# Kernel optimization log

Hardware: AMD Instinct MI355X
Metric: run time of the kernel (lower is better)

## Reference

```python
import jax, jax.numpy as jnp
import numpy as np
from jax import lax

H = 666
W = 666
EPS = 1e-5


def _conv(x, w, b):
    # NCHW conv, SAME padding, stride 1
    y = lax.conv_general_dilated(x, w, (1, 1), 'SAME',
                                 dimension_numbers=('NCHW', 'OIHW', 'NCHW'))
    return y + b[None, :, None, None]


def _bn2d(x, g, b):
    m = jnp.mean(x, (0, 2, 3), keepdims=True)
    v = jnp.var(x, (0, 2, 3), keepdims=True)
    return (x - m) * lax.rsqrt(v + EPS) * g[None, :, None, None] + b[None, :, None, None]


def _pool(x):
    return lax.reduce_window(x, -jnp.inf, lax.max, (1, 1, 2, 2), (1, 1, 2, 2), 'VALID')


def setup_inputs() -> dict:
    key = jax.random.key(0)
    ks = jax.random.split(key, 16)
    P, N, D = 20000, 32, 9

    def rn(k, shape, scale=0.05):
        return (jax.random.normal(k, shape, jnp.float32) * scale).astype(jnp.float32)

    return {
        'pillars': jax.random.normal(ks[0], (P, N, D), jnp.float32),
        'coords': jax.random.randint(ks[1], (P, 3), 0, 666, jnp.int64 if jax.config.jax_enable_x64 else jnp.int32),
        # PillarFeatureNet
        'lin_w': rn(ks[2], (64, 9)), 'lin_b': jnp.zeros((64,), jnp.float32),
        'pfn_g': jnp.ones((64,), jnp.float32), 'pfn_b': jnp.zeros((64,), jnp.float32),
        # Backbone
        'c1_w': rn(ks[3], (64, 64, 3, 3)), 'c1_b': jnp.zeros((64,), jnp.float32),
        'bn1_g': jnp.ones((64,), jnp.float32), 'bn1_b': jnp.zeros((64,), jnp.float32),
        'c2_w': rn(ks[4], (128, 64, 3, 3)), 'c2_b': jnp.zeros((128,), jnp.float32),
        'bn2_g': jnp.ones((128,), jnp.float32), 'bn2_b': jnp.zeros((128,), jnp.float32),
        # SSD head
        'h1_w': rn(ks[5], (256, 128, 3, 3)), 'h1_b': jnp.zeros((256,), jnp.float32),
        'hbn_g': jnp.ones((256,), jnp.float32), 'hbn_b': jnp.zeros((256,), jnp.float32),
        'hb_w': rn(ks[6], (21, 256, 3, 3)), 'hb_b': jnp.zeros((21,), jnp.float32),
        'hc_w': rn(ks[7], (3, 256, 3, 3)), 'hc_b': jnp.zeros((3,), jnp.float32),
    }


def reference(pillars, coords, lin_w, lin_b, pfn_g, pfn_b,
              c1_w, c1_b, bn1_g, bn1_b, c2_w, c2_b, bn2_g, bn2_b,
              h1_w, h1_b, hbn_g, hbn_b, hb_w, hb_b, hc_w, hc_b):
    P, N, D = pillars.shape
    # --- PillarFeatureNet: Linear -> BN1d (batch stats) -> ReLU -> max over points ---
    x = pillars.reshape(P * N, D) @ lin_w.T + lin_b           # [P*N, 64]
    m = jnp.mean(x, 0)
    v = jnp.var(x, 0)
    x = jax.nn.relu((x - m) * lax.rsqrt(v + EPS) * pfn_g + pfn_b)
    feats = jnp.max(x.reshape(P, N, -1), axis=1)              # [P, 64]

    # --- PseudoImageScatter: one vectorized scatter replacing the per-pillar loop ---
    y_idx = coords[:, 1]
    x_idx = coords[:, 2]
    valid = (y_idx >= 0) & (y_idx < H) & (x_idx >= 0) & (x_idx < W)
    y_idx = jnp.where(valid, y_idx, H)   # OOB -> dropped by scatter
    x_idx = jnp.where(valid, x_idx, W)
    img = jnp.zeros((64, H, W), feats.dtype).at[:, y_idx, x_idx].set(feats.T, mode='drop')
    img = img[None]                                           # [1, 64, H, W]

    # --- Backbone ---
    b1 = _pool(jax.nn.relu(_bn2d(_conv(img, c1_w, c1_b), bn1_g, bn1_b)))   # [1,64,333,333]
    b2 = _pool(jax.nn.relu(_bn2d(_conv(b1, c2_w, c2_b), bn2_g, bn2_b)))    # [1,128,166,166]

    # --- SSD head ---
    h = jax.nn.relu(_bn2d(_conv(b2, h1_w, h1_b), hbn_g, hbn_b))            # [1,256,166,166]
    bbox = _conv(h, hb_w, hb_b)                                            # [1,21,166,166]
    cls = _conv(h, hc_w, hc_b)                                             # [1,3,166,166]
    return (bbox, cls)
```

## Files before the change

### kernel.cpp

```cpp
#include <hip/hip_runtime.h>
#include <hip/hip_bf16.h>
#include <cstdint>
#include <cstddef>

#define BN_EPS 1e-5f

typedef short short8 __attribute__((ext_vector_type(8)));
typedef float float16 __attribute__((ext_vector_type(16)));
typedef unsigned short ushort_t;

__device__ __forceinline__ float bf2f(ushort_t u) {
  return __uint_as_float(((unsigned int)u) << 16);
}
__device__ __forceinline__ ushort_t f2bf(float f) {
  unsigned int u = __float_as_uint(f);
  u += 0x7FFFu + ((u >> 16) & 1u);
  return (ushort_t)(u >> 16);
}

__device__ __forceinline__ void gload16(const ushort_t* g, ushort_t* l) {
  __builtin_amdgcn_global_load_lds(
      (const __attribute__((address_space(1))) unsigned int*)g,
      (__attribute__((address_space(3))) unsigned int*)l, 16, 0, 0);
}


__global__ __launch_bounds__(512) void pillar_moments(
    const float* __restrict__ pillars, float* __restrict__ mom) {
  float S[9], M[45];
#pragma unroll
  for (int i = 0; i < 9; ++i) S[i] = 0.f;
#pragma unroll
  for (int i = 0; i < 45; ++i) M[i] = 0.f;
  const int t = blockIdx.x * 512 + threadIdx.x;
  const int NTH = 128 * 512;
  for (long r = t; r < 640000; r += NTH) {
    float x[9];
    const float* rp = pillars + r * 9;
#pragma unroll
    for (int d = 0; d < 9; ++d) x[d] = rp[d];
    int k = 0;
#pragma unroll
    for (int i = 0; i < 9; ++i) {
      S[i] += x[i];
#pragma unroll
      for (int j = i; j < 9; ++j) { M[k] += x[i] * x[j]; ++k; }
    }
  }
#pragma unroll
  for (int i = 0; i < 9; ++i)
#pragma unroll
    for (int o = 32; o > 0; o >>= 1) S[i] += __shfl_xor(S[i], o);
#pragma unroll
  for (int i = 0; i < 45; ++i)
#pragma unroll
    for (int o = 32; o > 0; o >>= 1) M[i] += __shfl_xor(M[i], o);
  __shared__ float red[8 * 54];
  int lane = threadIdx.x & 63, wv = threadIdx.x >> 6;
  if (lane == 0) {
#pragma unroll
    for (int i = 0; i < 9; ++i) red[wv * 54 + i] = S[i];
#pragma unroll
    for (int i = 0; i < 45; ++i) red[wv * 54 + 9 + i] = M[i];
  }
  __syncthreads();
  if (threadIdx.x < 54) {
    float s = 0.f;
#pragma unroll
    for (int w8 = 0; w8 < 8; ++w8) s += red[w8 * 54 + threadIdx.x];
    atomicAdd(&mom[threadIdx.x], s);
  }
}

__global__ void pfn_finalize(const float* __restrict__ mom,
                             const float* __restrict__ lin_w,
                             const float* __restrict__ lin_b,
                             const float* __restrict__ g, const float* __restrict__ b,
                             float* __restrict__ ss) {
  int c = threadIdx.x;
  double w[9], S[9];
#pragma unroll
  for (int d = 0; d < 9; ++d) {
    w[d] = (double)lin_w[c * 9 + d];
    S[d] = (double)mom[d];
  }
  double wS = 0.0;
#pragma unroll
  for (int d = 0; d < 9; ++d) wS += w[d] * S[d];
  double wMw = 0.0;
  int k = 0;
#pragma unroll
  for (int i = 0; i < 9; ++i)
#pragma unroll
    for (int j = i; j < 9; ++j) {
      double m = (double)mom[9 + k];
      wMw += (i == j ? 1.0 : 2.0) * w[i] * w[j] * m;
      ++k;
    }
  const double N = 640000.0;
  double bc = (double)lin_b[c];
  double mean = (wS + N * bc) / N;
  double ey2 = (wMw + 2.0 * bc * wS + N * bc * bc) / N;
  double var = ey2 - mean * mean;
  if (var < 0.0) var = 0.0;
  double inv = 1.0 / sqrt(var + (double)BN_EPS);
  double sc = (double)g[c] * inv;
  ss[c] = (float)sc;
  ss[c + 64] = (float)((double)b[c] - mean * sc);
}

__global__ __launch_bounds__(256) void pfn_feats(
    const float* __restrict__ pillars, const float* __restrict__ lin_w,
    const float* __restrict__ lin_b, const float* __restrict__ ss,
    ushort_t* __restrict__ feats) {
  __shared__ float s_p[1152];
  int tid = threadIdx.x;
  int c = tid & 63, pe = tid >> 6;
  long pb = (long)blockIdx.x * 4;
  for (int i = tid; i < 1152; i += 256) s_p[i] = pillars[pb * 288 + i];
  float w[9];
#pragma unroll
  for (int d = 0; d < 9; ++d) w[d] = lin_w[c * 9 + d];
  float bl = lin_b[c];
  float sc = ss[c], sh = ss[c + 64];
  __syncthreads();
  const float* pp = &s_p[pe * 288];
  float m = -1e30f;
#pragma unroll 4
  for (int n = 0; n < 32; ++n) {
    float y = bl;
#pragma unroll
    for (int d = 0; d < 9; ++d) y += pp[n * 9 + d] * w[d];
    float v = fmaxf(y * sc + sh, 0.f);
    m = fmaxf(m, v);
  }
  feats[(pb + pe) * 64 + c] = f2bf(m);
}


__global__ void scatter_winner(const int* __restrict__ coords, int* __restrict__ winner,
                               int P) {
  int p = blockIdx.x * 256 + threadIdx.x;
  if (p >= P) return;
  int y = coords[p * 3 + 1], x = coords[p * 3 + 2];
  if (y >= 0 && y < 666 && x >= 0 && x < 666) atomicMax(&winner[y * 666 + x], p);
}


__device__ __forceinline__ void prep_one(const float* __restrict__ w,
                                         ushort_t* __restrict__ w2, int C, int N,
                                         int Ntg, int chunks, int u) {
  int total = chunks * 9 * 2 * Ntg * 64;
  if (u >= total) return;
  int l = u & 63;
  int g = u >> 6;
  int ntg = g % Ntg;
  int g2 = g / Ntg;
  int s = g2 & 1;
  int g3 = g2 >> 1;
  int pos = g3 % 9;
  int cc = g3 / 9;
  int n = ntg * 32 + (l & 31);
  int c0 = cc * 32 + s * 16 + (l >> 5) * 8;
  ushort_t o8[8];
#pragma unroll
  for (int j = 0; j < 8; ++j) {
    int c = c0 + j;
    float v = (n < N && c < C) ? w[((size_t)n * C + c) * 9 + pos] : 0.f;
    o8[j] = f2bf(v);
  }
  *(uint4*)&w2[(size_t)u * 8] = *(const uint4*)o8;
}

__device__ __forceinline__ void prep_head_one(const float* __restrict__ hb,
                                              const float* __restrict__ hc,
                                              ushort_t* __restrict__ w2, int u) {
  int total = 8 * 9 * 2 * 64;
  if (u >= total) return;
  int l = u & 63;
  int g = u >> 6;
  int s = g & 1;
  int g3 = g >> 1;
  int pos = g3 % 9;
  int cc = g3 / 9;
  int n = l & 31;
  int c0 = cc * 32 + s * 16 + (l >> 5) * 8;
  ushort_t o8[8];
#pragma unroll
  for (int j = 0; j < 8; ++j) {
    int c = c0 + j;
    float v = 0.f;
    if (n < 21) v = hb[((size_t)n * 256 + c) * 9 + pos];
    else if (n < 24) v = hc[((size_t)(n - 21) * 256 + c) * 9 + pos];
    o8[j] = f2bf(v);
  }
  *(uint4*)&w2[(size_t)u * 8] = *(const uint4*)o8;
}

__global__ void prep_all(const float* __restrict__ c1_w, const float* __restrict__ c2_w,
                         const float* __restrict__ h1_w, const float* __restrict__ hb_w,
                         const float* __restrict__ hc_w, ushort_t* __restrict__ w2c1,
                         ushort_t* __restrict__ w2c2, ushort_t* __restrict__ w2h1,
                         ushort_t* __restrict__ w2hd) {
  int b = blockIdx.x;
  int t = threadIdx.x;
  if (b < 18) prep_one(c1_w, w2c1, 64, 64, 2, 2, b * 256 + t);
  else if (b < 54) prep_one(c2_w, w2c2, 64, 128, 4, 2, (b - 18) * 256 + t);
  else if (b < 198) prep_one(h1_w, w2h1, 128, 256, 8, 4, (b - 54) * 256 + t);
  else prep_head_one(hb_w, hc_w, w2hd, (b - 198) * 256 + t);
}


__global__ void bn_make_coefs(const float* __restrict__ acc, const float* __restrict__ g,
                              const float* __restrict__ b, float invN,
                              float* __restrict__ coef, int C) {
  int c = threadIdx.x;
  if (c >= C) return;
  float m = acc[c] * invN;
  float v = fmaxf(acc[c + 256] * invN - m * m, 0.f);
  float sc = g[c] * rsqrtf(v + BN_EPS);
  coef[c] = sc;
  coef[C + c] = b[c] - m * sc;
}


__global__ __launch_bounds__(256) void bnrelu(const ushort_t* __restrict__ inp,
                                              const float* __restrict__ coef, int C,
                                              int L8, ushort_t* __restrict__ outp) {
  __shared__ float sc[512];
  int tid = threadIdx.x;
  for (int i = tid; i < 2 * C; i += 256) sc[i] = coef[i];
  __syncthreads();
  int t = blockIdx.x * 256 + tid;
  if (t >= L8) return;
  size_t e0 = (size_t)t * 8;
  int c0 = (t << 3) & (C - 1);
  short8 v = *(const short8*)&inp[e0];
  const ushort_t* vp = (const ushort_t*)&v;
  ushort_t o[8];
#pragma unroll
  for (int j = 0; j < 8; ++j) {
    float x = bf2f(vp[j]);
    o[j] = f2bf(fmaxf(x * sc[c0 + j] + sc[C + c0 + j], 0.f));
  }
  *(uint4*)&outp[e0] = *(const uint4*)o;
}


template <int NT, int WAVES, bool GATHER, bool HEAD, bool STATS, bool POOL>
__global__ __launch_bounds__(WAVES * 64, 4) void conv_mfma(
    const ushort_t* __restrict__ in, const int* __restrict__ winner,
    const ushort_t* __restrict__ feats, const ushort_t* __restrict__ w2,
    const float* __restrict__ bias, const float* __restrict__ bias2,
    const ushort_t* __restrict__ zbuf, ushort_t* __restrict__ obf,
    float* __restrict__ hpart, float* __restrict__ statacc, int W, int H, int C,
    int nchunks, int Ntg) {
  constexpr int NTHREADS = WAVES * 64;
  constexpr int NPOS = (WAVES + 2) * 66;
  constexpr int IN_U4 = NPOS * 2;
  constexpr int W_U4 = 9 * NT * 64;
  constexpr int INIT = (IN_U4 + NTHREADS - 1) / NTHREADS;
  constexpr int WIT = (W_U4 + NTHREADS - 1) / NTHREADS;
  __shared__ ushort_t s_in[2][IN_U4 * 8];
  __shared__ ushort_t s_w[2][W_U4 * 8];
  const int tid = threadIdx.x;
  const int lane = tid & 63, wv = tid >> 6;
  const int lc = lane & 31, lh = lane >> 5;
  const int x0 = blockIdx.x * 64, y0 = blockIdx.y * WAVES;
  const int z = blockIdx.z;
  const int cc0 = HEAD ? z * nchunks : 0;
  const int z_oc = HEAD ? 0 : z;

  int pc[2][3];
#pragma unroll
  for (int Mt = 0; Mt < 2; ++Mt)
#pragma unroll
    for (int kx = 0; kx < 3; ++kx) {
      int col = Mt * 32 + kx + lc;
      pc[Mt][kx] = col * 16 + (lh ^ (col & 1)) * 8;
    }

  const ushort_t* isrc[INIT];
#pragma unroll
  for (int it = 0; it < INIT; ++it) {
    isrc[it] = zbuf;
    int d = it * NTHREADS + tid;
    if (d < IN_U4) {
      int p = d >> 1, g = d & 1;
      int r = p / 66, col = p - r * 66;
      int cg = g ^ (col & 1);
      int gy = y0 - 1 + r, gx = x0 - 1 + col;
      if (gy >= 0 && gy < H && gx >= 0 && gx < W) {
        if (GATHER) {
          int pw = winner[gy * 666 + gx];
          if (pw >= 0) isrc[it] = feats + pw * 64 + cg * 8;
        } else {
          isrc[it] = in + (size_t)(gy * W + gx) * C + cg * 8;
        }
      }
    }
  }
  int wof[WIT];
#pragma unroll
  for (int it = 0; it < WIT; ++it) {
    wof[it] = 0;
    int d = it * NTHREADS + tid;
    if (d < W_U4) {
      int grp = d >> 6, l16 = d & 63;
      int pos = grp / NT, nt = grp % NT;
      wof[it] = (pos * 2 * Ntg + z_oc * NT + nt) * 512 + l16 * 8;
    }
  }

  float bv[NT];
#pragma unroll
  for (int nt = 0; nt < NT; ++nt) {
    if (HEAD) {
      bv[nt] = (z == 0) ? (lc < 21 ? bias[lc] : (lc < 24 ? bias2[lc - 21] : 0.f)) : 0.f;
    } else {
      bv[nt] = bias[(z * NT + nt) * 32 + lc];
    }
  }
  float16 acc[2][NT];
#pragma unroll
  for (int Mt = 0; Mt < 2; ++Mt)
#pragma unroll
    for (int nt = 0; nt < NT; ++nt)
#pragma unroll
      for (int r = 0; r < 16; ++r) acc[Mt][nt][r] = bv[nt];

  auto stage = [&](int ph, int b) {
    int ccg = cc0 + (ph >> 1), sh = ph & 1;
    int coff = ccg * 32 + sh * 16;
#pragma unroll
    for (int it = 0; it < INIT; ++it) {
      int d = it * NTHREADS + tid;
      if (d < IN_U4)
        gload16(isrc[it] + coff, &s_in[b][(size_t)(it * NTHREADS + wv * 64) * 8]);
    }
    int wbase = (ccg * 18 + sh) * Ntg * 512;
#pragma unroll
    for (int it = 0; it < WIT; ++it) {
      int d = it * NTHREADS + tid;
      if (d < W_U4)
        gload16(w2 + wbase + wof[it], &s_w[b][(size_t)(it * NTHREADS + wv * 64) * 8]);
    }
  };

  auto compute_phase = [&](int b) {
#pragma unroll
    for (int ky = 0; ky < 3; ++ky) {
      const ushort_t* rowp = &s_in[b][(wv + ky) * (66 * 16)];
#pragma unroll
      for (int kx = 0; kx < 3; ++kx) {
        const int pos = ky * 3 + kx;
        short8 Bf[NT];
#pragma unroll
        for (int nt = 0; nt < NT; ++nt)
          Bf[nt] = *(const short8*)&s_w[b][(pos * NT + nt) * 512 + lane * 8];
#pragma unroll
        for (int Mt = 0; Mt < 2; ++Mt) {
          short8 Af = *(const short8*)&rowp[pc[Mt][kx]];
#pragma unroll
          for (int nt = 0; nt < NT; ++nt)
            acc[Mt][nt] =
                __builtin_amdgcn_mfma_f32_32x32x16_bf16(Af, Bf[nt], acc[Mt][nt], 0, 0, 0);
        }
      }
    }
  };

  const int nph = nchunks * 2;
  stage(0, 0);
  for (int ph = 0; ph < nph; ++ph) {
    asm volatile("s_waitcnt vmcnt(0)\n\ts_barrier" ::: "memory");
    if (ph + 1 < nph) stage(ph + 1, (ph + 1) & 1);
    __builtin_amdgcn_s_setprio(1);
    compute_phase(ph & 1);
    __builtin_amdgcn_s_setprio(0);
  }

  const int y = y0 + wv;
  const bool yok = (y < H);
  const int Ntot = Ntg * 32;

  if (HEAD) {
    if (yok) {
      float* hp = hpart + (size_t)z * (size_t)(H * W) * 32;
#pragma unroll
      for (int Mt = 0; Mt < 2; ++Mt)
#pragma unroll
        for (int r = 0; r < 16; ++r) {
          int m = (r & 3) + 8 * (r >> 2) + 4 * lh;
          int x = x0 + Mt * 32 + m;
          if (x < W) {
            size_t sp = (size_t)y * W + x;
            hp[sp * 32 + lc] = acc[Mt][0][r];
          }
        }
    }
    return;
  }

  if (!POOL) {
    if (yok) {
#pragma unroll
      for (int Mt = 0; Mt < 2; ++Mt)
#pragma unroll
        for (int r = 0; r < 16; ++r) {
          int m = (r & 3) + 8 * (r >> 2) + 4 * lh;
          int x = x0 + Mt * 32 + m;
          if (x < W) {
            size_t sp = (size_t)y * W + x;
#pragma unroll
            for (int nt = 0; nt < NT; ++nt) {
              int oc = (z * NT + nt) * 32 + lc;
              obf[sp * Ntot + oc] = f2bf(acc[Mt][nt][r]);
            }
          }
        }
    }
  }

  if (STATS) {
    float s1[NT], s2[NT];
#pragma unroll
    for (int nt = 0; nt < NT; ++nt) { s1[nt] = 0.f; s2[nt] = 0.f; }
    if (yok) {
#pragma unroll
      for (int Mt = 0; Mt < 2; ++Mt)
#pragma unroll
        for (int r = 0; r < 16; ++r) {
          int m = (r & 3) + 8 * (r >> 2) + 4 * lh;
          int x = x0 + Mt * 32 + m;
          if (x < W) {
#pragma unroll
            for (int nt = 0; nt < NT; ++nt) {
              float v = acc[Mt][nt][r];
              s1[nt] += v;
              s2[nt] += v * v;
            }
          }
        }
    }
#pragma unroll
    for (int nt = 0; nt < NT; ++nt) {
      s1[nt] += __shfl_xor(s1[nt], 32);
      s2[nt] += __shfl_xor(s2[nt], 32);
    }
    __syncthreads();
    float* red = (float*)s_in;
    if (lh == 0) {
#pragma unroll
      for (int nt = 0; nt < NT; ++nt) {
        red[(wv * NT + nt) * 32 + lc] = s1[nt];
        red[WAVES * NT * 32 + (wv * NT + nt) * 32 + lc] = s2[nt];
      }
    }
    __syncthreads();
    if (wv == 0 && lh == 0) {
#pragma unroll
      for (int nt = 0; nt < NT; ++nt) {
        float a = 0.f, b = 0.f;
#pragma unroll
        for (int w8 = 0; w8 < WAVES; ++w8) {
          a += red[(w8 * NT + nt) * 32 + lc];
          b += red[WAVES * NT * 32 + (w8 * NT + nt) * 32 + lc];
        }
        int ch = (z * NT + nt) * 32 + lc;
        atomicAdd(&statacc[ch], a);
        atomicAdd(&statacc[ch + 256], b);
      }
    }
  }

  if (POOL) {
    const int OWp = W >> 1, OHp = H >> 1;
    float hm[2][NT][8];
#pragma unroll
    for (int Mt = 0; Mt < 2; ++Mt)
#pragma unroll
      for (int nt = 0; nt < NT; ++nt)
#pragma unroll
        for (int i = 0; i < 8; ++i)
          hm[Mt][nt][i] = fmaxf(acc[Mt][nt][2 * i], acc[Mt][nt][2 * i + 1]);
    __syncthreads();
    float* pl = (float*)s_in;
    if (wv & 1) {
#pragma unroll
      for (int Mt = 0; Mt < 2; ++Mt)
#pragma unroll
        for (int nt = 0; nt < NT; ++nt)
#pragma unroll
          for (int i = 0; i < 8; ++i)
            pl[((((wv >> 1) * 2 + Mt) * NT + nt) * 8 + i) * 64 + lane] = hm[Mt][nt][i];
    }
    __syncthreads();
    if (!(wv & 1)) {
      int oy = (y0 + wv) >> 1;
      if (oy < OHp) {
#pragma unroll
        for (int Mt = 0; Mt < 2; ++Mt)
#pragma unroll
          for (int i = 0; i < 8; ++i) {
            int pxl = Mt * 16 + (i >> 1) * 4 + (i & 1) + 2 * lh;
            int ox = (x0 >> 1) + pxl;
            if (ox < OWp) {
#pragma unroll
              for (int nt = 0; nt < NT; ++nt) {
                float v = fmaxf(
                    hm[Mt][nt][i],
                    pl[((((wv >> 1) * 2 + Mt) * NT + nt) * 8 + i) * 64 + lane]);
                int oc = (z * NT + nt) * 32 + lc;
                obf[((size_t)oy * OWp + ox) * Ntot + oc] = f2bf(v);
              }
            }
          }
      }
    }
  }
}


__global__ __launch_bounds__(256) void head_reduce(const float* __restrict__ hp,
                                                   float* __restrict__ out, int HW,
                                                   int nz) {
  __shared__ float t[256 * 33];
  int tid = threadIdx.x;
  int sp0 = blockIdx.x * 256;
  int lim = (HW - sp0) * 32;
#pragma unroll 4
  for (int i = 0; i < 32; ++i) {
    int e = i * 256 + tid;
    float s = 0.f;
    if (e < lim) {
      size_t gidx = (size_t)sp0 * 32 + e;
      for (int z = 0; z < nz; ++z) s += hp[(size_t)z * HW * 32 + gidx];
    }
    t[(e >> 5) * 33 + (e & 31)] = s;
  }
  __syncthreads();
  int sp = sp0 + tid;
  if (sp < HW) {
#pragma unroll
    for (int ch = 0; ch < 24; ++ch)
      out[(size_t)ch * HW + sp] = t[tid * 33 + ch];
  }
}


extern "C" void kernel_launch(void* const* d_in, const int* in_sizes, int n_in,
                              void* d_out, int out_size, void* d_ws, size_t ws_size,
                              hipStream_t stream) {
  (void)in_sizes; (void)n_in; (void)out_size; (void)ws_size;
  const float* pillars = (const float*)d_in[0];
  const int* coords = (const int*)d_in[1];
  const float* lin_w = (const float*)d_in[2];
  const float* lin_b = (const float*)d_in[3];
  const float* pfn_g = (const float*)d_in[4];
  const float* pfn_b = (const float*)d_in[5];
  const float* c1_w = (const float*)d_in[6];
  const float* c1_b = (const float*)d_in[7];
  const float* bn1_g = (const float*)d_in[8];
  const float* bn1_b = (const float*)d_in[9];
  const float* c2_w = (const float*)d_in[10];
  const float* c2_b = (const float*)d_in[11];
  const float* bn2_g = (const float*)d_in[12];
  const float* bn2_b = (const float*)d_in[13];
  const float* h1_w = (const float*)d_in[14];
  const float* h1_b = (const float*)d_in[15];
  const float* hbn_g = (const float*)d_in[16];
  const float* hbn_b = (const float*)d_in[17];
  const float* hb_w = (const float*)d_in[18];
  const float* hb_b = (const float*)d_in[19];
  const float* hc_w = (const float*)d_in[20];
  const float* hc_b = (const float*)d_in[21];
  float* out = (float*)d_out;

  char* ws = (char*)d_ws;
  float* mom     = (float*)(ws + 0);
  float* pfn_ss  = (float*)(ws + 512);
  float* bn_acc1 = (float*)(ws + 1024);
  float* bn_acc2 = (float*)(ws + 3072);
  float* bn_acc3 = (float*)(ws + 5120);
  float* coef1   = (float*)(ws + 7168);
  float* coef2   = (float*)(ws + 7680);
  float* coef3   = (float*)(ws + 8704);
  ushort_t* zbuf = (ushort_t*)(ws + 10752);
  int* winner    = (int*)(ws + 11264);
  ushort_t* feats  = (ushort_t*)(ws + 1785600);
  ushort_t* c1p    = (ushort_t*)(ws + 4345600);
  ushort_t* c2a    = (ushort_t*)(ws + 4345600);
  ushort_t* c2p    = (ushort_t*)(ws + 18539392);
  ushort_t* h1out  = (ushort_t*)(ws + 25593728);
  ushort_t* w2c1   = (ushort_t*)(ws + 39702400);
  ushort_t* w2c2   = (ushort_t*)(ws + 39776128);
  ushort_t* w2h1   = (ushort_t*)(ws + 39923584);
  ushort_t* w2hd   = (ushort_t*)(ws + 40513408);
  float* hpart     = (float*)(ws + 40660864);
  ushort_t* c1a    = (ushort_t*)(ws + 54769536);
  ushort_t* h1a    = (ushort_t*)(ws + 54769536);

  const int HW3 = 166 * 166;

  hipMemsetAsync(ws, 0, 11264, stream);
  hipMemsetAsync(winner, 0xFF, 1774224, stream);

  prep_all<<<234, 256, 0, stream>>>(c1_w, c2_w, h1_w, hb_w, hc_w, w2c1, w2c2, w2h1,
                                    w2hd);

  pillar_moments<<<128, 512, 0, stream>>>(pillars, mom);
  pfn_finalize<<<1, 64, 0, stream>>>(mom, lin_w, lin_b, pfn_g, pfn_b, pfn_ss);
  pfn_feats<<<5000, 256, 0, stream>>>(pillars, lin_w, lin_b, pfn_ss, feats);

  scatter_winner<<<(20000 + 255) / 256, 256, 0, stream>>>(coords, winner, 20000);

  conv_mfma<2, 8, true, false, true, true><<<dim3(11, 84, 1), 512, 0, stream>>>(
      nullptr, winner, feats, w2c1, c1_b, nullptr, zbuf, c1p, nullptr, bn_acc1, 666,
      666, 64, 2, 2);
  bn_make_coefs<<<1, 64, 0, stream>>>(bn_acc1, bn1_g, bn1_b, 1.f / 443556.f, coef1, 64);

  bnrelu<<<(887112 + 255) / 256, 256, 0, stream>>>(c1p, coef1, 64, 887112, c1a);

  conv_mfma<2, 8, false, false, true, true><<<dim3(6, 42, 2), 512, 0, stream>>>(
      c1a, nullptr, nullptr, w2c2, c2_b, nullptr, zbuf, c2p, nullptr, bn_acc2, 333, 333,
      64, 2, 4);
  bn_make_coefs<<<1, 128, 0, stream>>>(bn_acc2, bn2_g, bn2_b, 1.f / 110889.f, coef2, 128);

  bnrelu<<<(440896 + 255) / 256, 256, 0, stream>>>(c2p, coef2, 128, 440896, c2a);

  conv_mfma<2, 4, false, false, true, false><<<dim3(3, 42, 4), 256, 0, stream>>>(
      c2a, nullptr, nullptr, w2h1, h1_b, nullptr, zbuf, h1out, nullptr, bn_acc3, 166,
      166, 128, 4, 8);
  bn_make_coefs<<<1, 256, 0, stream>>>(bn_acc3, hbn_g, hbn_b, 1.f / 27556.f, coef3, 256);

  bnrelu<<<(881792 + 255) / 256, 256, 0, stream>>>(h1out, coef3, 256, 881792, h1a);

  conv_mfma<1, 4, false, true, false, false><<<dim3(3, 42, 4), 256, 0, stream>>>(
      h1a, nullptr, nullptr, w2hd, hb_b, hc_b, zbuf, nullptr, hpart, nullptr, 166,
      166, 256, 2, 1);
  head_reduce<<<(HW3 + 255) / 256, 256, 0, stream>>>(hpart, out, HW3, 4);
}
```

Measured before the change: 323.0 us.

## Fuse BN+ReLU into conv input staging and merge small launches

```diff
diff --git a/kernel.cpp b/kernel.cpp
--- a/kernel.cpp
+++ b/kernel.cpp
@@ -22,128 +22,6 @@
   __builtin_amdgcn_global_load_lds(
       (const __attribute__((address_space(1))) unsigned int*)g,
       (__attribute__((address_space(3))) unsigned int*)l, 16, 0, 0);
-}
-
-
-__global__ __launch_bounds__(512) void pillar_moments(
-    const float* __restrict__ pillars, float* __restrict__ mom) {
-  float S[9], M[45];
-#pragma unroll
-  for (int i = 0; i < 9; ++i) S[i] = 0.f;
-#pragma unroll
-  for (int i = 0; i < 45; ++i) M[i] = 0.f;
-  const int t = blockIdx.x * 512 + threadIdx.x;
-  const int NTH = 128 * 512;
-  for (long r = t; r < 640000; r += NTH) {
-    float x[9];
-    const float* rp = pillars + r * 9;
-#pragma unroll
-    for (int d = 0; d < 9; ++d) x[d] = rp[d];
-    int k = 0;
-#pragma unroll
-    for (int i = 0; i < 9; ++i) {
-      S[i] += x[i];
-#pragma unroll
-      for (int j = i; j < 9; ++j) { M[k] += x[i] * x[j]; ++k; }
-    }
-  }
-#pragma unroll
-  for (int i = 0; i < 9; ++i)
-#pragma unroll
-    for (int o = 32; o > 0; o >>= 1) S[i] += __shfl_xor(S[i], o);
-#pragma unroll
-  for (int i = 0; i < 45; ++i)
-#pragma unroll
-    for (int o = 32; o > 0; o >>= 1) M[i] += __shfl_xor(M[i], o);
-  __shared__ float red[8 * 54];
-  int lane = threadIdx.x & 63, wv = threadIdx.x >> 6;
-  if (lane == 0) {
-#pragma unroll
-    for (int i = 0; i < 9; ++i) red[wv * 54 + i] = S[i];
-#pragma unroll
-    for (int i = 0; i < 45; ++i) red[wv * 54 + 9 + i] = M[i];
-  }
-  __syncthreads();
-  if (threadIdx.x < 54) {
-    float s = 0.f;
-#pragma unroll
-    for (int w8 = 0; w8 < 8; ++w8) s += red[w8 * 54 + threadIdx.x];
-    atomicAdd(&mom[threadIdx.x], s);
-  }
-}
-
-__global__ void pfn_finalize(const float* __restrict__ mom,
-                             const float* __restrict__ lin_w,
-                             const float* __restrict__ lin_b,
-                             const float* __restrict__ g, const float* __restrict__ b,
-                             float* __restrict__ ss) {
-  int c = threadIdx.x;
-  double w[9], S[9];
-#pragma unroll
-  for (int d = 0; d < 9; ++d) {
-    w[d] = (double)lin_w[c * 9 + d];
-    S[d] = (double)mom[d];
-  }
-  double wS = 0.0;
-#pragma unroll
-  for (int d = 0; d < 9; ++d) wS += w[d] * S[d];
-  double wMw = 0.0;
-  int k = 0;
-#pragma unroll
-  for (int i = 0; i < 9; ++i)
-#pragma unroll
-    for (int j = i; j < 9; ++j) {
-      double m = (double)mom[9 + k];
-      wMw += (i == j ? 1.0 : 2.0) * w[i] * w[j] * m;
-      ++k;
-    }
-  const double N = 640000.0;
-  double bc = (double)lin_b[c];
-  double mean = (wS + N * bc) / N;
-  double ey2 = (wMw + 2.0 * bc * wS + N * bc * bc) / N;
-  double var = ey2 - mean * mean;
-  if (var < 0.0) var = 0.0;
-  double inv = 1.0 / sqrt(var + (double)BN_EPS);
-  double sc = (double)g[c] * inv;
-  ss[c] = (float)sc;
-  ss[c + 64] = (float)((double)b[c] - mean * sc);
-}
-
-__global__ __launch_bounds__(256) void pfn_feats(
-    const float* __restrict__ pillars, const float* __restrict__ lin_w,
-    const float* __restrict__ lin_b, const float* __restrict__ ss,
-    ushort_t* __restrict__ feats) {
-  __shared__ float s_p[1152];
-  int tid = threadIdx.x;
-  int c = tid & 63, pe = tid >> 6;
-  long pb = (long)blockIdx.x * 4;
-  for (int i = tid; i < 1152; i += 256) s_p[i] = pillars[pb * 288 + i];
-  float w[9];
-#pragma unroll
-  for (int d = 0; d < 9; ++d) w[d] = lin_w[c * 9 + d];
-  float bl = lin_b[c];
-  float sc = ss[c], sh = ss[c + 64];
-  __syncthreads();
-  const float* pp = &s_p[pe * 288];
-  float m = -1e30f;
-#pragma unroll 4
-  for (int n = 0; n < 32; ++n) {
-    float y = bl;
-#pragma unroll
-    for (int d = 0; d < 9; ++d) y += pp[n * 9 + d] * w[d];
-    float v = fmaxf(y * sc + sh, 0.f);
-    m = fmaxf(m, v);
-  }
-  feats[(pb + pe) * 64 + c] = f2bf(m);
-}
-
-
-__global__ void scatter_winner(const int* __restrict__ coords, int* __restrict__ winner,
-                               int P) {
-  int p = blockIdx.x * 256 + threadIdx.x;
-  if (p >= P) return;
-  int y = coords[p * 3 + 1], x = coords[p * 3 + 2];
-  if (y >= 0 && y < 666 && x >= 0 && x < 666) atomicMax(&winner[y * 666 + x], p);
 }
 
 
@@ -197,79 +75,163 @@
   *(uint4*)&w2[(size_t)u * 8] = *(const uint4*)o8;
 }
 
-__global__ void prep_all(const float* __restrict__ c1_w, const float* __restrict__ c2_w,
-                         const float* __restrict__ h1_w, const float* __restrict__ hb_w,
-                         const float* __restrict__ hc_w, ushort_t* __restrict__ w2c1,
-                         ushort_t* __restrict__ w2c2, ushort_t* __restrict__ w2h1,
-                         ushort_t* __restrict__ w2hd) {
+
+__global__ __launch_bounds__(256) void fused_prep(
+    const float* __restrict__ c1_w, const float* __restrict__ c2_w,
+    const float* __restrict__ h1_w, const float* __restrict__ hb_w,
+    const float* __restrict__ hc_w, ushort_t* __restrict__ w2c1,
+    ushort_t* __restrict__ w2c2, ushort_t* __restrict__ w2h1,
+    ushort_t* __restrict__ w2hd, const float* __restrict__ pillars,
+    float* __restrict__ mom) {
   int b = blockIdx.x;
   int t = threadIdx.x;
-  if (b < 18) prep_one(c1_w, w2c1, 64, 64, 2, 2, b * 256 + t);
-  else if (b < 54) prep_one(c2_w, w2c2, 64, 128, 4, 2, (b - 18) * 256 + t);
-  else if (b < 198) prep_one(h1_w, w2h1, 128, 256, 8, 4, (b - 54) * 256 + t);
-  else prep_head_one(hb_w, hc_w, w2hd, (b - 198) * 256 + t);
-}
-
-
-__global__ void bn_make_coefs(const float* __restrict__ acc, const float* __restrict__ g,
-                              const float* __restrict__ b, float invN,
-                              float* __restrict__ coef, int C) {
+  if (b < 18) { prep_one(c1_w, w2c1, 64, 64, 2, 2, b * 256 + t); return; }
+  if (b < 54) { prep_one(c2_w, w2c2, 64, 128, 4, 2, (b - 18) * 256 + t); return; }
+  if (b < 198) { prep_one(h1_w, w2h1, 128, 256, 8, 4, (b - 54) * 256 + t); return; }
+  if (b < 234) { prep_head_one(hb_w, hc_w, w2hd, (b - 198) * 256 + t); return; }
+  float S[9], M[45];
+#pragma unroll
+  for (int i = 0; i < 9; ++i) S[i] = 0.f;
+#pragma unroll
+  for (int i = 0; i < 45; ++i) M[i] = 0.f;
+  const int t0 = (b - 234) * 256 + t;
+  const int NTH = 256 * 256;
+  for (long r = t0; r < 640000; r += NTH) {
+    float x[9];
+    const float* rp = pillars + r * 9;
+#pragma unroll
+    for (int d = 0; d < 9; ++d) x[d] = rp[d];
+    int k = 0;
+#pragma unroll
+    for (int i = 0; i < 9; ++i) {
+      S[i] += x[i];
+#pragma unroll
+      for (int j = i; j < 9; ++j) { M[k] += x[i] * x[j]; ++k; }
+    }
+  }
+#pragma unroll
+  for (int i = 0; i < 9; ++i)
+#pragma unroll
+    for (int o = 32; o > 0; o >>= 1) S[i] += __shfl_xor(S[i], o);
+#pragma unroll
+  for (int i = 0; i < 45; ++i)
+#pragma unroll
+    for (int o = 32; o > 0; o >>= 1) M[i] += __shfl_xor(M[i], o);
+  __shared__ float red[4 * 54];
+  int lane = t & 63, wv = t >> 6;
+  if (lane == 0) {
+#pragma unroll
+    for (int i = 0; i < 9; ++i) red[wv * 54 + i] = S[i];
+#pragma unroll
+    for (int i = 0; i < 45; ++i) red[wv * 54 + 9 + i] = M[i];
+  }
+  __syncthreads();
+  if (t < 54) {
+    float s = 0.f;
+#pragma unroll
+    for (int w4 = 0; w4 < 4; ++w4) s += red[w4 * 54 + t];
+    atomicAdd(&mom[t], s);
+  }
+}
+
+
+__global__ void pfn_finalize(const float* __restrict__ mom,
+                             const float* __restrict__ lin_w,
+                             const float* __restrict__ lin_b,
+                             const float* __restrict__ g, const float* __restrict__ b,
+                             float* __restrict__ ss) {
   int c = threadIdx.x;
-  if (c >= C) return;
-  float m = acc[c] * invN;
-  float v = fmaxf(acc[c + 256] * invN - m * m, 0.f);
-  float sc = g[c] * rsqrtf(v + BN_EPS);
-  coef[c] = sc;
-  coef[C + c] = b[c] - m * sc;
-}
-
-
-__global__ __launch_bounds__(256) void bnrelu(const ushort_t* __restrict__ inp,
-                                              const float* __restrict__ coef, int C,
-                                              int L8, ushort_t* __restrict__ outp) {
-  __shared__ float sc[512];
+  double w[9], S[9];
+#pragma unroll
+  for (int d = 0; d < 9; ++d) {
+    w[d] = (double)lin_w[c * 9 + d];
+    S[d] = (double)mom[d];
+  }
+  double wS = 0.0;
+#pragma unroll
+  for (int d = 0; d < 9; ++d) wS += w[d] * S[d];
+  double wMw = 0.0;
+  int k = 0;
+#pragma unroll
+  for (int i = 0; i < 9; ++i)
+#pragma unroll
+    for (int j = i; j < 9; ++j) {
+      double m = (double)mom[9 + k];
+      wMw += (i == j ? 1.0 : 2.0) * w[i] * w[j] * m;
+      ++k;
+    }
+  const double N = 640000.0;
+  double bc = (double)lin_b[c];
+  double mean = (wS + N * bc) / N;
+  double ey2 = (wMw + 2.0 * bc * wS + N * bc * bc) / N;
+  double var = ey2 - mean * mean;
+  if (var < 0.0) var = 0.0;
+  double inv = 1.0 / sqrt(var + (double)BN_EPS);
+  double sc = (double)g[c] * inv;
+  ss[c] = (float)sc;
+  ss[c + 64] = (float)((double)b[c] - mean * sc);
+}
+
+
+__global__ __launch_bounds__(256) void feats_scatter(
+    const float* __restrict__ pillars, const float* __restrict__ lin_w,
+    const float* __restrict__ lin_b, const float* __restrict__ ss,
+    ushort_t* __restrict__ feats, const int* __restrict__ coords,
+    int* __restrict__ winner) {
   int tid = threadIdx.x;
-  for (int i = tid; i < 2 * C; i += 256) sc[i] = coef[i];
-  __syncthreads();
-  int t = blockIdx.x * 256 + tid;
-  if (t >= L8) return;
-  size_t e0 = (size_t)t * 8;
-  int c0 = (t << 3) & (C - 1);
-  short8 v = *(const short8*)&inp[e0];
-  const ushort_t* vp = (const ushort_t*)&v;
-  ushort_t o[8];
-#pragma unroll
-  for (int j = 0; j < 8; ++j) {
-    float x = bf2f(vp[j]);
-    o[j] = f2bf(fmaxf(x * sc[c0 + j] + sc[C + c0 + j], 0.f));
-  }
-  *(uint4*)&outp[e0] = *(const uint4*)o;
-}
-
-
-template <int NT, int WAVES, bool GATHER, bool HEAD, bool STATS, bool POOL>
-__global__ __launch_bounds__(WAVES * 64, 4) void conv_mfma(
-    const ushort_t* __restrict__ in, const int* __restrict__ winner,
-    const ushort_t* __restrict__ feats, const ushort_t* __restrict__ w2,
-    const float* __restrict__ bias, const float* __restrict__ bias2,
+  if (blockIdx.x < 5000) {
+    __shared__ float s_p[1152];
+    int c = tid & 63, pe = tid >> 6;
+    long pb = (long)blockIdx.x * 4;
+    for (int i = tid; i < 1152; i += 256) s_p[i] = pillars[pb * 288 + i];
+    float w[9];
+#pragma unroll
+    for (int d = 0; d < 9; ++d) w[d] = lin_w[c * 9 + d];
+    float bl = lin_b[c];
+    float sc = ss[c], sh = ss[c + 64];
+    __syncthreads();
+    const float* pp = &s_p[pe * 288];
+    float m = -1e30f;
+#pragma unroll 4
+    for (int n = 0; n < 32; ++n) {
+      float y = bl;
+#pragma unroll
+      for (int d = 0; d < 9; ++d) y += pp[n * 9 + d] * w[d];
+      float v = fmaxf(y * sc + sh, 0.f);
+      m = fmaxf(m, v);
+    }
+    feats[(pb + pe) * 64 + c] = f2bf(m);
+  } else {
+    int p = (blockIdx.x - 5000) * 256 + tid;
+    if (p >= 20000) return;
+    int y = coords[p * 3 + 1], x = coords[p * 3 + 2];
+    if (y >= 0 && y < 666 && x >= 0 && x < 666) atomicMax(&winner[y * 666 + x], p);
+  }
+}
+
+
+template <int NT, int WAVES>
+__global__ __launch_bounds__(WAVES * 64, 4) void conv_g(
+    const int* __restrict__ winner, const ushort_t* __restrict__ feats,
+    const ushort_t* __restrict__ w2, const float* __restrict__ bias,
     const ushort_t* __restrict__ zbuf, ushort_t* __restrict__ obf,
-    float* __restrict__ hpart, float* __restrict__ statacc, int W, int H, int C,
-    int nchunks, int Ntg) {
+    float* __restrict__ statacc, int W, int H, int nchunks, int Ntg) {
   constexpr int NTHREADS = WAVES * 64;
   constexpr int NPOS = (WAVES + 2) * 66;
   constexpr int IN_U4 = NPOS * 2;
   constexpr int W_U4 = 9 * NT * 64;
   constexpr int INIT = (IN_U4 + NTHREADS - 1) / NTHREADS;
   constexpr int WIT = (W_U4 + NTHREADS - 1) / NTHREADS;
-  __shared__ ushort_t s_in[2][IN_U4 * 8];
+  constexpr int IN_SLOTS = ((IN_U4 + 63) / 64) * 64;
+  __shared__ ushort_t s_in[2][IN_SLOTS * 8];
   __shared__ ushort_t s_w[2][W_U4 * 8];
+  __shared__ ushort_t s_junk[512];
   const int tid = threadIdx.x;
   const int lane = tid & 63, wv = tid >> 6;
   const int lc = lane & 31, lh = lane >> 5;
   const int x0 = blockIdx.x * 64, y0 = blockIdx.y * WAVES;
   const int z = blockIdx.z;
-  const int cc0 = HEAD ? z * nchunks : 0;
-  const int z_oc = HEAD ? 0 : z;
+  const int z_oc = z;
 
   int pc[2][3];
 #pragma unroll
@@ -291,12 +253,8 @@
       int cg = g ^ (col & 1);
       int gy = y0 - 1 + r, gx = x0 - 1 + col;
       if (gy >= 0 && gy < H && gx >= 0 && gx < W) {
-        if (GATHER) {
-          int pw = winner[gy * 666 + gx];
-          if (pw >= 0) isrc[it] = feats + pw * 64 + cg * 8;
-        } else {
-          isrc[it] = in + (size_t)(gy * W + gx) * C + cg * 8;
-        }
+        int pw = winner[gy * 666 + gx];
+        if (pw >= 0) isrc[it] = feats + pw * 64 + cg * 8;
       }
     }
   }
@@ -314,13 +272,7 @@
 
   float bv[NT];
 #pragma unroll
-  for (int nt = 0; nt < NT; ++nt) {
-    if (HEAD) {
-      bv[nt] = (z == 0) ? (lc < 21 ? bias[lc] : (lc < 24 ? bias2[lc - 21] : 0.f)) : 0.f;
-    } else {
-      bv[nt] = bias[(z * NT + nt) * 32 + lc];
-    }
-  }
+  for (int nt = 0; nt < NT; ++nt) bv[nt] = bias[(z * NT + nt) * 32 + lc];
   float16 acc[2][NT];
 #pragma unroll
   for (int Mt = 0; Mt < 2; ++Mt)
@@ -330,15 +282,15 @@
       for (int r = 0; r < 16; ++r) acc[Mt][nt][r] = bv[nt];
 
   auto stage = [&](int ph, int b) {
-    int ccg = cc0 + (ph >> 1), sh = ph & 1;
-    int coff = ccg * 32 + sh * 16;
+    int ccg = ph >> 1, sh2 = ph & 1;
+    int coff = ccg * 32 + sh2 * 16;
 #pragma unroll
     for (int it = 0; it < INIT; ++it) {
       int d = it * NTHREADS + tid;
       if (d < IN_U4)
         gload16(isrc[it] + coff, &s_in[b][(size_t)(it * NTHREADS + wv * 64) * 8]);
     }
-    int wbase = (ccg * 18 + sh) * Ntg * 512;
+    int wbase = (ccg * 18 + sh2) * Ntg * 512;
 #pragma unroll
     for (int it = 0; it < WIT; ++it) {
       int d = it * NTHREADS + tid;
@@ -384,45 +336,7 @@
   const bool yok = (y < H);
   const int Ntot = Ntg * 32;
 
-  if (HEAD) {
-    if (yok) {
-      float* hp = hpart + (size_t)z * (size_t)(H * W) * 32;
-#pragma unroll
-      for (int Mt = 0; Mt < 2; ++Mt)
-#pragma unroll
-        for (int r = 0; r < 16; ++r) {
-          int m = (r & 3) + 8 * (r >> 2) + 4 * lh;
-          int x = x0 + Mt * 32 + m;
-          if (x < W) {
-            size_t sp = (size_t)y * W + x;
-            hp[sp * 32 + lc] = acc[Mt][0][r];
-          }
-        }
-    }
-    return;
-  }
-
-  if (!POOL) {
-    if (yok) {
-#pragma unroll
-      for (int Mt = 0; Mt < 2; ++Mt)
-#pragma unroll
-        for (int r = 0; r < 16; ++r) {
-          int m = (r & 3) + 8 * (r >> 2) + 4 * lh;
-          int x = x0 + Mt * 32 + m;
-          if (x < W) {
-            size_t sp = (size_t)y * W + x;
-#pragma unroll
-            for (int nt = 0; nt < NT; ++nt) {
-              int oc = (z * NT + nt) * 32 + lc;
-              obf[sp * Ntot + oc] = f2bf(acc[Mt][nt][r]);
-            }
-          }
-        }
-    }
-  }
-
-  if (STATS) {
+  {
     float s1[NT], s2[NT];
 #pragma unroll
     for (int nt = 0; nt < NT; ++nt) { s1[nt] = 0.f; s2[nt] = 0.f; }
@@ -474,7 +388,7 @@
     }
   }
 
-  if (POOL) {
+  {
     const int OWp = W >> 1, OHp = H >> 1;
     float hm[2][NT][8];
 #pragma unroll
@@ -522,29 +436,283 @@
 }
 
 
-__global__ __launch_bounds__(256) void head_reduce(const float* __restrict__ hp,
-                                                   float* __restrict__ out, int HW,
-                                                   int nz) {
-  __shared__ float t[256 * 33];
-  int tid = threadIdx.x;
-  int sp0 = blockIdx.x * 256;
-  int lim = (HW - sp0) * 32;
-#pragma unroll 4
-  for (int i = 0; i < 32; ++i) {
-    int e = i * 256 + tid;
-    float s = 0.f;
-    if (e < lim) {
-      size_t gidx = (size_t)sp0 * 32 + e;
-      for (int z = 0; z < nz; ++z) s += hp[(size_t)z * HW * 32 + gidx];
-    }
-    t[(e >> 5) * 33 + (e & 31)] = s;
-  }
-  __syncthreads();
-  int sp = sp0 + tid;
-  if (sp < HW) {
-#pragma unroll
-    for (int ch = 0; ch < 24; ++ch)
-      out[(size_t)ch * HW + sp] = t[tid * 33 + ch];
+template <int NT, int WAVES, bool HEAD, bool STATS, bool POOL>
+__global__ __launch_bounds__(WAVES * 64, WAVES == 8 ? 4 : 3) void conv_s(
+    const ushort_t* __restrict__ in, const ushort_t* __restrict__ w2,
+    const float* __restrict__ bias, const float* __restrict__ bias2,
+    const float* __restrict__ bnacc, const float* __restrict__ bng,
+    const float* __restrict__ bnb, float invN, ushort_t* __restrict__ obf,
+    float* __restrict__ hout, float* __restrict__ statacc, int W, int H, int C,
+    int nchunks, int Ntg) {
+  constexpr int NTHREADS = WAVES * 64;
+  __shared__ ushort_t s_in[(WAVES + 2) * 66 * 32];
+  __shared__ ushort_t s_w[9 * 2 * NT * 512];
+  __shared__ float s_coef[512];
+  const int tid = threadIdx.x;
+  const int lane = tid & 63, wv = tid >> 6;
+  const int lc = lane & 31, lh = lane >> 5;
+  const int x0 = blockIdx.x * 64, y0 = blockIdx.y * WAVES;
+  const int z = blockIdx.z;
+  const int cc0 = HEAD ? z * nchunks : 0;
+  const int z_oc = HEAD ? 0 : z;
+
+  if (tid < C) {
+    float m = bnacc[tid] * invN;
+    float v = fmaxf(bnacc[tid + 256] * invN - m * m, 0.f);
+    float sc = bng[tid] * rsqrtf(v + BN_EPS);
+    s_coef[tid] = sc;
+    s_coef[C + tid] = bnb[tid] - m * sc;
+  }
+
+  int pc[2][2][3];
+#pragma unroll
+  for (int s = 0; s < 2; ++s)
+#pragma unroll
+    for (int Mt = 0; Mt < 2; ++Mt)
+#pragma unroll
+      for (int kx = 0; kx < 3; ++kx) {
+        int col = Mt * 32 + kx + lc;
+        int q = (2 * s + lh) ^ ((col >> 1) & 3);
+        pc[s][Mt][kx] = col * 32 + q * 8;
+      }
+
+  const int sg = tid & 3;
+  const int tpos = tid >> 2;
+  constexpr int TPOS = NTHREADS / 4;
+  constexpr int NPOS = (WAVES + 2) * 66;
+  constexpr int NIT = (NPOS + TPOS - 1) / TPOS;
+  int ldst[NIT], gsrc[NIT];
+#pragma unroll
+  for (int it = 0; it < NIT; ++it) {
+    ldst[it] = -1;
+    gsrc[it] = -1;
+    int p = tpos + it * TPOS;
+    if (p < NPOS) {
+      int r = p / 66, col = p - r * 66;
+      int f = sg ^ ((col >> 1) & 3);
+      ldst[it] = (r * 66 + col) * 32 + f * 8;
+      int gy = y0 - 1 + r, gx = x0 - 1 + col;
+      if (gy >= 0 && gy < H && gx >= 0 && gx < W)
+        gsrc[it] = (gy * W + gx) * C + sg * 8;
+    }
+  }
+
+  float bv[NT];
+#pragma unroll
+  for (int nt = 0; nt < NT; ++nt) {
+    if (HEAD) {
+      bv[nt] = (z == 0) ? (lc < 21 ? bias[lc] : (lc < 24 ? bias2[lc - 21] : 0.f)) : 0.f;
+    } else {
+      bv[nt] = bias[(z * NT + nt) * 32 + lc];
+    }
+  }
+  float16 acc[2][NT];
+#pragma unroll
+  for (int Mt = 0; Mt < 2; ++Mt)
+#pragma unroll
+    for (int nt = 0; nt < NT; ++nt)
+#pragma unroll
+      for (int r = 0; r < 16; ++r) acc[Mt][nt][r] = bv[nt];
+
+  for (int cc = 0; cc < nchunks; ++cc) {
+    const int ccg = cc0 + cc;
+    __syncthreads();
+    {
+      float sc8[8], sh8[8];
+      int ch = ccg * 32 + sg * 8;
+      float4 a0 = *(const float4*)&s_coef[ch];
+      float4 a1 = *(const float4*)&s_coef[ch + 4];
+      float4 b0 = *(const float4*)&s_coef[C + ch];
+      float4 b1 = *(const float4*)&s_coef[C + ch + 4];
+      sc8[0] = a0.x; sc8[1] = a0.y; sc8[2] = a0.z; sc8[3] = a0.w;
+      sc8[4] = a1.x; sc8[5] = a1.y; sc8[6] = a1.z; sc8[7] = a1.w;
+      sh8[0] = b0.x; sh8[1] = b0.y; sh8[2] = b0.z; sh8[3] = b0.w;
+      sh8[4] = b1.x; sh8[5] = b1.y; sh8[6] = b1.z; sh8[7] = b1.w;
+#pragma unroll
+      for (int it = 0; it < NIT; ++it) {
+        if (ldst[it] < 0) continue;
+        ushort_t v8[8] = {0, 0, 0, 0, 0, 0, 0, 0};
+        if (gsrc[it] >= 0) {
+          uint4 raw = *(const uint4*)&in[gsrc[it] + ccg * 32];
+          const ushort_t* rp = (const ushort_t*)&raw;
+#pragma unroll
+          for (int j = 0; j < 8; ++j)
+            v8[j] = f2bf(fmaxf(bf2f(rp[j]) * sc8[j] + sh8[j], 0.f));
+        }
+        *(uint4*)&s_in[ldst[it]] = *(const uint4*)v8;
+      }
+    }
+    {
+      const int NW = NT * 1152;
+      for (int u = tid; u < NW; u += NTHREADS) {
+        int l16 = u & 63, grp = u >> 6;
+        int nt = grp % NT, ps = grp / NT;
+        const ushort_t* src =
+            w2 + ((size_t)((ccg * 18 + ps) * Ntg + z_oc * NT + nt) * 64 + l16) * 8;
+        *(uint4*)&s_w[(size_t)u * 8] = *(const uint4*)src;
+      }
+    }
+    __syncthreads();
+#pragma unroll
+    for (int ky = 0; ky < 3; ++ky) {
+      int rowoff = (wv + ky) * (66 * 32);
+#pragma unroll
+      for (int kx = 0; kx < 3; ++kx) {
+        const int pos = ky * 3 + kx;
+#pragma unroll
+        for (int s = 0; s < 2; ++s) {
+          short8 Bf[NT];
+#pragma unroll
+          for (int nt = 0; nt < NT; ++nt)
+            Bf[nt] = *(const short8*)&s_w[((pos * 2 + s) * NT + nt) * 512 + lane * 8];
+#pragma unroll
+          for (int Mt = 0; Mt < 2; ++Mt) {
+            short8 Af = *(const short8*)&s_in[rowoff + pc[s][Mt][kx]];
+#pragma unroll
+            for (int nt = 0; nt < NT; ++nt)
+              acc[Mt][nt] =
+                  __builtin_amdgcn_mfma_f32_32x32x16_bf16(Af, Bf[nt], acc[Mt][nt], 0, 0, 0);
+          }
+        }
+      }
+    }
+  }
+
+  const int y = y0 + wv;
+  const bool yok = (y < H);
+  const int Ntot = Ntg * 32;
+
+  if (HEAD) {
+    if (yok && lc < 24) {
+      float* op = hout + (size_t)lc * (size_t)(H * W);
+#pragma unroll
+      for (int Mt = 0; Mt < 2; ++Mt)
+#pragma unroll
+        for (int r = 0; r < 16; ++r) {
+          int m = (r & 3) + 8 * (r >> 2) + 4 * lh;
+          int x = x0 + Mt * 32 + m;
+          if (x < W) atomicAdd(&op[(size_t)y * W + x], acc[Mt][0][r]);
+        }
+    }
+    return;
+  }
+
+  if (!POOL) {
+    if (yok) {
+#pragma unroll
+      for (int Mt = 0; Mt < 2; ++Mt)
+#pragma unroll
+        for (int r = 0; r < 16; ++r) {
+          int m = (r & 3) + 8 * (r >> 2) + 4 * lh;
+          int x = x0 + Mt * 32 + m;
+          if (x < W) {
+            size_t sp = (size_t)y * W + x;
+#pragma unroll
+            for (int nt = 0; nt < NT; ++nt) {
+              int oc = (z * NT + nt) * 32 + lc;
+              obf[sp * Ntot + oc] = f2bf(acc[Mt][nt][r]);
+            }
+          }
+        }
+    }
+  }
+
+  if (STATS) {
+    float s1[NT], s2[NT];
+#pragma unroll
+    for (int nt = 0; nt < NT; ++nt) { s1[nt] = 0.f; s2[nt] = 0.f; }
+    if (yok) {
+#pragma unroll
+      for (int Mt = 0; Mt < 2; ++Mt)
+#pragma unroll
+        for (int r = 0; r < 16; ++r) {
+          int m = (r & 3) + 8 * (r >> 2) + 4 * lh;
+          int x = x0 + Mt * 32 + m;
+          if (x < W) {
+#pragma unroll
+            for (int nt = 0; nt < NT; ++nt) {
+              float v = acc[Mt][nt][r];
+              s1[nt] += v;
+              s2[nt] += v * v;
+            }
+          }
+        }
+    }
+#pragma unroll
+    for (int nt = 0; nt < NT; ++nt) {
+      s1[nt] += __shfl_xor(s1[nt], 32);
+      s2[nt] += __shfl_xor(s2[nt], 32);
+    }
+    __syncthreads();
+    float* red = (float*)s_in;
+    if (lh == 0) {
+#pragma unroll
+      for (int nt = 0; nt < NT; ++nt) {
+        red[(wv * NT + nt) * 32 + lc] = s1[nt];
+        red[WAVES * NT * 32 + (wv * NT + nt) * 32 + lc] = s2[nt];
+      }
+    }
+    __syncthreads();
+    if (wv == 0 && lh == 0) {
+#pragma unroll
+      for (int nt = 0; nt < NT; ++nt) {
+        float a = 0.f, b = 0.f;
+#pragma unroll
+        for (int w8 = 0; w8 < WAVES; ++w8) {
+          a += red[(w8 * NT + nt) * 32 + lc];
+          b += red[WAVES * NT * 32 + (w8 * NT + nt) * 32 + lc];
+        }
+        int ch = (z * NT + nt) * 32 + lc;
+        atomicAdd(&statacc[ch], a);
+        atomicAdd(&statacc[ch + 256], b);
+      }
+    }
+  }
+
+  if (POOL) {
+    const int OWp = W >> 1, OHp = H >> 1;
+    float hm[2][NT][8];
+#pragma unroll
+    for (int Mt = 0; Mt < 2; ++Mt)
+#pragma unroll
+      for (int nt = 0; nt < NT; ++nt)
+#pragma unroll
+        for (int i = 0; i < 8; ++i)
+          hm[Mt][nt][i] = fmaxf(acc[Mt][nt][2 * i], acc[Mt][nt][2 * i + 1]);
+    __syncthreads();
+    float* pl = (float*)s_in;
+    if (wv & 1) {
+#pragma unroll
+      for (int Mt = 0; Mt < 2; ++Mt)
+#pragma unroll
+        for (int nt = 0; nt < NT; ++nt)
+#pragma unroll
+          for (int i = 0; i < 8; ++i)
+            pl[((((wv >> 1) * 2 + Mt) * NT + nt) * 8 + i) * 64 + lane] = hm[Mt][nt][i];
+    }
+    __syncthreads();
+    if (!(wv & 1)) {
+      int oy = (y0 + wv) >> 1;
+      if (oy < OHp) {
+#pragma unroll
+        for (int Mt = 0; Mt < 2; ++Mt)
+#pragma unroll
+          for (int i = 0; i < 8; ++i) {
+            int pxl = Mt * 16 + (i >> 1) * 4 + (i & 1) + 2 * lh;
+            int ox = (x0 >> 1) + pxl;
+            if (ox < OWp) {
+#pragma unroll
+              for (int nt = 0; nt < NT; ++nt) {
+                float v = fmaxf(
+                    hm[Mt][nt][i],
+                    pl[((((wv >> 1) * 2 + Mt) * NT + nt) * 8 + i) * 64 + lane]);
+                int oc = (z * NT + nt) * 32 + lc;
+                obf[((size_t)oy * OWp + ox) * Ntot + oc] = f2bf(v);
+              }
+            }
+          }
+      }
+    }
   }
 }
 
@@ -583,61 +751,40 @@
   float* bn_acc1 = (float*)(ws + 1024);
   float* bn_acc2 = (float*)(ws + 3072);
   float* bn_acc3 = (float*)(ws + 5120);
-  float* coef1   = (float*)(ws + 7168);
-  float* coef2   = (float*)(ws + 7680);
-  float* coef3   = (float*)(ws + 8704);
   ushort_t* zbuf = (ushort_t*)(ws + 10752);
   int* winner    = (int*)(ws + 11264);
   ushort_t* feats  = (ushort_t*)(ws + 1785600);
   ushort_t* c1p    = (ushort_t*)(ws + 4345600);
-  ushort_t* c2a    = (ushort_t*)(ws + 4345600);
   ushort_t* c2p    = (ushort_t*)(ws + 18539392);
   ushort_t* h1out  = (ushort_t*)(ws + 25593728);
   ushort_t* w2c1   = (ushort_t*)(ws + 39702400);
   ushort_t* w2c2   = (ushort_t*)(ws + 39776128);
   ushort_t* w2h1   = (ushort_t*)(ws + 39923584);
   ushort_t* w2hd   = (ushort_t*)(ws + 40513408);
-  float* hpart     = (float*)(ws + 40660864);
-  ushort_t* c1a    = (ushort_t*)(ws + 54769536);
-  ushort_t* h1a    = (ushort_t*)(ws + 54769536);
-
-  const int HW3 = 166 * 166;
 
   hipMemsetAsync(ws, 0, 11264, stream);
   hipMemsetAsync(winner, 0xFF, 1774224, stream);
-
-  prep_all<<<234, 256, 0, stream>>>(c1_w, c2_w, h1_w, hb_w, hc_w, w2c1, w2c2, w2h1,
-                                    w2hd);
-
-  pillar_moments<<<128, 512, 0, stream>>>(pillars, mom);
+  hipMemsetAsync(out, 0, 24 * 27556 * 4, stream);
+
+  fused_prep<<<490, 256, 0, stream>>>(c1_w, c2_w, h1_w, hb_w, hc_w, w2c1, w2c2,
+                                      w2h1, w2hd, pillars, mom);
   pfn_finalize<<<1, 64, 0, stream>>>(mom, lin_w, lin_b, pfn_g, pfn_b, pfn_ss);
-  pfn_feats<<<5000, 256, 0, stream>>>(pillars, lin_w, lin_b, pfn_ss, feats);
-
-  scatter_winner<<<(20000 + 255) / 256, 256, 0, stream>>>(coords, winner, 20000);
-
-  conv_mfma<2, 8, true, false, true, true><<<dim3(11, 84, 1), 512, 0, stream>>>(
-      nullptr, winner, feats, w2c1, c1_b, nullptr, zbuf, c1p, nullptr, bn_acc1, 666,
-      666, 64, 2, 2);
-  bn_make_coefs<<<1, 64, 0, stream>>>(bn_acc1, bn1_g, bn1_b, 1.f / 443556.f, coef1, 64);
-
-  bnrelu<<<(887112 + 255) / 256, 256, 0, stream>>>(c1p, coef1, 64, 887112, c1a);
-
-  conv_mfma<2, 8, false, false, true, true><<<dim3(6, 42, 2), 512, 0, stream>>>(
-      c1a, nullptr, nullptr, w2c2, c2_b, nullptr, zbuf, c2p, nullptr, bn_acc2, 333, 333,
-      64, 2, 4);
-  bn_make_coefs<<<1, 128, 0, stream>>>(bn_acc2, bn2_g, bn2_b, 1.f / 110889.f, coef2, 128);
-
-  bnrelu<<<(440896 + 255) / 256, 256, 0, stream>>>(c2p, coef2, 128, 440896, c2a);
-
-  conv_mfma<2, 4, false, false, true, false><<<dim3(3, 42, 4), 256, 0, stream>>>(
-      c2a, nullptr, nullptr, w2h1, h1_b, nullptr, zbuf, h1out, nullptr, bn_acc3, 166,
-      166, 128, 4, 8);
-  bn_make_coefs<<<1, 256, 0, stream>>>(bn_acc3, hbn_g, hbn_b, 1.f / 27556.f, coef3, 256);
-
-  bnrelu<<<(881792 + 255) / 256, 256, 0, stream>>>(h1out, coef3, 256, 881792, h1a);
-
-  conv_mfma<1, 4, false, true, false, false><<<dim3(3, 42, 4), 256, 0, stream>>>(
-      h1a, nullptr, nullptr, w2hd, hb_b, hc_b, zbuf, nullptr, hpart, nullptr, 166,
-      166, 256, 2, 1);
-  head_reduce<<<(HW3 + 255) / 256, 256, 0, stream>>>(hpart, out, HW3, 4);
-}
+
+  feats_scatter<<<5079, 256, 0, stream>>>(pillars, lin_w, lin_b, pfn_ss, feats,
+                                          coords, winner);
+
+  conv_g<2, 8><<<dim3(11, 84, 1), 512, 0, stream>>>(
+      winner, feats, w2c1, c1_b, zbuf, c1p, bn_acc1, 666, 666, 2, 2);
+
+  conv_s<2, 8, false, true, true><<<dim3(6, 42, 2), 512, 0, stream>>>(
+      c1p, w2c2, c2_b, nullptr, bn_acc1, bn1_g, bn1_b, 1.f / 443556.f, c2p, nullptr,
+      bn_acc2, 333, 333, 64, 2, 4);
+
+  conv_s<2, 4, false, true, false><<<dim3(3, 42, 4), 256, 0, stream>>>(
+      c2p, w2h1, h1_b, nullptr, bn_acc2, bn2_g, bn2_b, 1.f / 110889.f, h1out, nullptr,
+      bn_acc3, 166, 166, 128, 4, 8);
+
+  conv_s<1, 4, true, false, false><<<dim3(3, 42, 4), 256, 0, stream>>>(
+      h1out, w2hd, hb_b, hc_b, bn_acc3, hbn_g, hbn_b, 1.f / 27556.f, nullptr, out,
+      nullptr, 166, 166, 256, 2, 1);
+}
```

New measurement: 354.9 us. 1.1x slower.
